# Kernel tuning notes

Measured on AMD Instinct MI355X. Metric: run time of the kernel, lower is better.

## Reference

```python
import jax, jax.numpy as jnp
import numpy as np

B, N = 2, 200
IMG = 2048
NC = 4                    # node concepts ('Is*')
NODE_CH = NC * 256        # 1024
EC = 3                    # edge concepts minus 'HigherPri'
AC = 4                    # actions
BBOX_MAX = 1024.0
E = N * (N - 1)

# static fully-connected directed edge list (src=i, dst=j, i!=j), row-major order
_ii, _jj = np.meshgrid(np.arange(N), np.arange(N), indexing='ij')
_m = _ii != _jj
SRC = jnp.asarray(_ii[_m])
DST = jnp.asarray(_jj[_m])


def _lin(k, fin, fout):
    kw, kb = jax.random.split(k)
    s = 1.0 / np.sqrt(fin)
    return (jax.random.uniform(kw, (fin, fout), jnp.float32, -s, s),
            jax.random.uniform(kb, (fout,), jnp.float32, -s, s))


def setup_inputs():
    ks = jax.random.split(jax.random.key(0), 16)
    p = {}
    p['roi_features'] = jax.random.normal(ks[0], (B, N, IMG), jnp.float32)
    p['batch_bboxes'] = jax.random.uniform(ks[1], (B, N, 4), jnp.float32) * BBOX_MAX
    p['batch_directions'] = jax.random.normal(ks[2], (B, N, 4), jnp.float32)
    p['batch_priorities'] = jax.random.normal(ks[3], (B, N), jnp.float32)
    p['w1'], p['b1'] = _lin(ks[4], IMG, 512)
    p['w2'], p['b2'] = _lin(ks[5], 512, 256)
    p['w3'], p['b3'] = _lin(ks[6], 256, NODE_CH)
    p['wi'], p['bi'] = _lin(ks[7], NODE_CH, NC)
    p['we1'], p['be1'] = _lin(ks[8], 16, 256)
    p['we2'], p['be2'] = _lin(ks[9], 256, 64)
    p['we3'], p['be3'] = _lin(ks[10], 64, EC)
    p['wp1'], p['bp1'] = _lin(ks[11], EC + 1, 128)
    p['wp2'], p['bp2'] = _lin(ks[12], 128, NODE_CH * AC)
    p['root_w'], _ = _lin(ks[13], NODE_CH, AC)
    _, p['root_b'] = _lin(ks[14], NODE_CH, AC)
    return p


def reference(roi_features, batch_bboxes, batch_directions, batch_priorities,
              w1, b1, w2, b2, w3, b3, wi, bi,
              we1, be1, we2, be2, we3, be3,
              wp1, bp1, wp2, bp2, root_w, root_b):
    # node concept embedding MLP: [B,N,IMG] -> [B,N,NODE_CH]
    h = jax.nn.relu(roi_features @ w1 + b1)
    h = jax.nn.relu(h @ w2 + b2)
    node_concepts = h @ w3 + b3
    node_concepts_explicit = jax.nn.sigmoid(node_concepts @ wi + bi)

    # pairwise attributes for all directed edges (same ordering as torch masks)
    node_attr = jnp.concatenate([batch_bboxes / BBOX_MAX, batch_directions], -1)  # [B,N,8]
    pair = jnp.concatenate([node_attr[:, SRC], node_attr[:, DST]], -1)            # [B,E,16]
    eh = jax.nn.relu(pair @ we1 + be1)
    eh = jax.nn.relu(eh @ we2 + be2)
    edge_attributes = jax.nn.sigmoid(eh @ we3 + be3)                              # [B,E,EC]
    higher_pri = (batch_priorities[:, SRC] > batch_priorities[:, DST]).astype(jnp.float32)
    edge_attributes = jnp.concatenate([edge_attributes, higher_pri[..., None]], -1)  # [B,E,EC+1]

    # NNConv on graph 0: per-edge weight matrix, gather-matmul-scatter
    x = node_concepts[0]                 # [N, NODE_CH]
    e = edge_attributes[0]               # [E, EC+1]
    w = jax.nn.relu(e @ wp1 + bp1) @ wp2 + bp2
    w = w.reshape(E, NODE_CH, AC)        # [E, NODE_CH, AC]
    msg = jnp.einsum('ei,eio->eo', x[SRC], w)          # [E, AC]
    agg = jax.ops.segment_sum(msg, DST, num_segments=N)  # [N, AC]
    next_actions = agg + x @ root_w + root_b
    return (next_actions, node_concepts_explicit[0], edge_attributes[0])
```

## Files before the change

### kernel.cpp

```cpp
#include <hip/hip_runtime.h>
#include <math.h>

#define NN 200
#define ETOT 39800

typedef float float4v __attribute__((ext_vector_type(4)));
typedef short short8 __attribute__((ext_vector_type(8)));

__device__ __forceinline__ float sigf(float x) { return 1.0f / (1.0f + expf(-x)); }

__device__ __forceinline__ unsigned short f2b(float f) {
  unsigned u = __float_as_uint(f);
  u += 0x7fffu + ((u >> 16) & 1u);
  return (unsigned short)(u >> 16);
}
__device__ __forceinline__ float b2f16(unsigned short u) {
  return __uint_as_float(((unsigned)u) << 16);
}

__global__ __launch_bounds__(256) void k_L1(
    const float* __restrict__ roi, const float* __restrict__ w1, const float* __restrict__ b1,
    const float* __restrict__ wp2, const float* __restrict__ w3,
    const float* __restrict__ wi, const float* __restrict__ rootw, const float* __restrict__ bp2,
    const float* __restrict__ b3, const float* __restrict__ w2, const float* __restrict__ we2,
    const float* __restrict__ bbox, const float* __restrict__ dir,
    const float* __restrict__ we1, const float* __restrict__ be1, const float* __restrict__ wp1,
    unsigned short* __restrict__ h1, unsigned short* __restrict__ Gm, float* __restrict__ G12f,
    float* __restrict__ Pm, float* __restrict__ Qm,
    unsigned short* __restrict__ we2T, unsigned short* __restrict__ w2T,
    float* __restrict__ wp1T, float* __restrict__ gvec, float* __restrict__ bcat) {
  __shared__ __align__(16) char sm[16640];
  const int b = blockIdx.x, tid = threadIdx.x;
  const int lane = tid & 63, wv = tid >> 6, mr = lane & 15, quad = lane >> 4;

  if (b < 416) {
    const int m0 = (b % 13) * 16, n0 = (b / 13) * 16;
    const int arow = min(m0 + mr, 199);
    const float* Ap = roi + (size_t)arow * 2048 + wv * 512 + quad * 8;
    const float* Bp0 = w1 + n0 + mr;
    float4v acc = {0.f, 0.f, 0.f, 0.f};
    for (int ks = 0; ks < 16; ++ks) {
      float4v a0 = *(const float4v*)(Ap + ks * 32);
      float4v a1 = *(const float4v*)(Ap + ks * 32 + 4);
      short8 af, bf;
      af[0]=f2b(a0[0]); af[1]=f2b(a0[1]); af[2]=f2b(a0[2]); af[3]=f2b(a0[3]);
      af[4]=f2b(a1[0]); af[5]=f2b(a1[1]); af[6]=f2b(a1[2]); af[7]=f2b(a1[3]);
      const float* Bp = Bp0 + (size_t)(wv * 512 + ks * 32 + quad * 8) * 512;
#pragma unroll
      for (int t8 = 0; t8 < 8; ++t8) bf[t8] = f2b(Bp[(size_t)t8 * 512]);
      acc = __builtin_amdgcn_mfma_f32_16x16x32_bf16(af, bf, acc, 0, 0, 0);
    }
    float (*red)[16][17] = (float (*)[16][17])sm;
#pragma unroll
    for (int r = 0; r < 4; ++r) red[wv][quad * 4 + r][mr] = acc[r];
    __syncthreads();
    const int row = tid >> 4, col = tid & 15;
    float v = red[0][row][col] + red[1][row][col] + red[2][row][col] + red[3][row][col] + b1[n0 + col];
    h1[(size_t)(m0 + row) * 512 + n0 + col] = f2b(fmaxf(v, 0.f));
  } else if (b < 928) {
    const int t = b - 416;
    const int j0 = (t % 32) * 16, c0 = (t / 32) * 16;
    const int j = j0 + mr;
    const float* Aw = wp2 + (size_t)(j >> 2) * 4096 + (j & 3);
    const float* Bp0 = w3 + (size_t)(c0 + mr) * 1024;
    float4v acc = {0.f, 0.f, 0.f, 0.f};
    for (int ks = 0; ks < 8; ++ks) {
      const int i0 = wv * 256 + ks * 32 + quad * 8;
      short8 af, bf;
#pragma unroll
      for (int t8 = 0; t8 < 8; ++t8) af[t8] = f2b(Aw[4 * (i0 + t8)]);
      float4v b0 = *(const float4v*)(Bp0 + i0);
      float4v b1v = *(const float4v*)(Bp0 + i0 + 4);
      bf[0]=f2b(b0[0]); bf[1]=f2b(b0[1]); bf[2]=f2b(b0[2]); bf[3]=f2b(b0[3]);
      bf[4]=f2b(b1v[0]); bf[5]=f2b(b1v[1]); bf[6]=f2b(b1v[2]); bf[7]=f2b(b1v[3]);
      acc = __builtin_amdgcn_mfma_f32_16x16x32_bf16(af, bf, acc, 0, 0, 0);
    }
    float (*red)[16][17] = (float (*)[16][17])sm;
#pragma unroll
    for (int r = 0; r < 4; ++r) red[wv][quad * 4 + r][mr] = acc[r];
    __syncthreads();
    const int row = tid >> 4, col = tid & 15;
    float v = red[0][row][col] + red[1][row][col] + red[2][row][col] + red[3][row][col];
    Gm[(size_t)(j0 + row) * 256 + c0 + col] = f2b(v);
  } else if (b < 1184) {
    const int c = b - 928;
    float s[12] = {};
#pragma unroll
    for (int ii = 0; ii < 4; ++ii) {
      int i = tid + ii * 256;
      float xv = w3[(size_t)c * 1024 + i];
      float4v wi4 = ((const float4v*)wi)[i];
      float4v rw4 = ((const float4v*)rootw)[i];
      float4v bp4 = ((const float4v*)bp2)[i];
#pragma unroll
      for (int q = 0; q < 4; ++q) {
        s[q] += xv * wi4[q]; s[4 + q] += xv * rw4[q]; s[8 + q] += xv * bp4[q];
      }
    }
    float (*part)[12] = (float (*)[12])sm;
#pragma unroll
    for (int r = 0; r < 12; ++r) {
      float v = s[r];
#pragma unroll
      for (int off = 32; off > 0; off >>= 1) v += __shfl_down(v, off, 64);
      if (lane == 0) part[wv][r] = v;
    }
    __syncthreads();
    if (tid < 12) G12f[c * 12 + tid] = part[0][tid] + part[1][tid] + part[2][tid] + part[3][tid];
  } else if (b < 1384) {
    const int n = b - 1184, c = tid;
    float a[8];
#pragma unroll
    for (int r = 0; r < 4; ++r) a[r] = bbox[n * 4 + r] * (1.0f / 1024.0f);
#pragma unroll
    for (int r = 0; r < 4; ++r) a[4 + r] = dir[n * 4 + r];
    float p = be1[c], q = 0.0f;
#pragma unroll
    for (int r = 0; r < 8; ++r) {
      p += a[r] * we1[r * 256 + c];
      q += a[r] * we1[(8 + r) * 256 + c];
    }
    Pm[n * 256 + c] = p;
    Qm[n * 256 + c] = q;
  } else if (b < 1400) {
    const int f = (b - 1384) * 256 + tid;
    const int c = f >> 6, k0 = (f & 63) * 4;
#pragma unroll
    for (int q = 0; q < 4; ++q)
      we2T[c * 256 + k0 + q] = f2b(we2[(k0 + q) * 64 + c]);
  } else if (b < 1432) {
    float (*lds)[65] = (float (*)[65])sm;
    const int t = b - 1400;
    const int kt = t % 8, nt = t / 8;
#pragma unroll 4
    for (int i = 0; i < 16; ++i) {
      int idx = tid + i * 256;
      int r = idx >> 6, c = idx & 63;
      lds[r][c] = w2[(size_t)(kt * 64 + r) * 256 + nt * 64 + c];
    }
    __syncthreads();
#pragma unroll 4
    for (int i = 0; i < 16; ++i) {
      int idx = tid + i * 256;
      int r = idx >> 6, c = idx & 63;
      w2T[(size_t)(nt * 64 + r) * 512 + kt * 64 + c] = f2b(lds[c][r]);
    }
  } else if (b < 1440) {
    const int j = (b - 1432) * 64 + (tid >> 2), p = tid & 3;
    const float* src = wp2 + (size_t)(j >> 2) * 4096 + (j & 3);
    float v = 0.f;
    for (int t = 0; t < 256; ++t) {
      int i = p + 4 * t;
      v += b3[i] * src[4 * i];
    }
    v += __shfl_down(v, 2, 4);
    v += __shfl_down(v, 1, 4);
    if (p == 0) gvec[j] = v;
  } else if (b == 1440) {
    if (tid < 128) {
      float4v v = {wp1[tid], wp1[128 + tid], wp1[256 + tid], wp1[384 + tid]};
      ((float4v*)wp1T)[tid] = v;
    }
  } else {
    float s[12] = {};
#pragma unroll
    for (int ii = 0; ii < 4; ++ii) {
      int i = tid + ii * 256;
      float xv = b3[i];
      float4v wi4 = ((const float4v*)wi)[i];
      float4v rw4 = ((const float4v*)rootw)[i];
      float4v bp4 = ((const float4v*)bp2)[i];
#pragma unroll
      for (int q = 0; q < 4; ++q) {
        s[q] += xv * wi4[q]; s[4 + q] += xv * rw4[q]; s[8 + q] += xv * bp4[q];
      }
    }
    float (*part)[12] = (float (*)[12])sm;
#pragma unroll
    for (int r = 0; r < 12; ++r) {
      float v = s[r];
#pragma unroll
      for (int off = 32; off > 0; off >>= 1) v += __shfl_down(v, off, 64);
      if (lane == 0) part[wv][r] = v;
    }
    __syncthreads();
    if (tid < 12) bcat[tid] = part[0][tid] + part[1][tid] + part[2][tid] + part[3][tid];
  }
}

__global__ __launch_bounds__(256) void k_L2(const unsigned short* __restrict__ h1,
                                            const unsigned short* __restrict__ w2T,
                                            const float* __restrict__ b2,
                                            unsigned short* __restrict__ h2) {
  __shared__ float red[4][16][17];
  const int tid = threadIdx.x, lane = tid & 63, wv = tid >> 6;
  const int m0 = (blockIdx.x % 13) * 16, n0 = (blockIdx.x / 13) * 16;
  const int mr = lane & 15, quad = lane >> 4;
  const unsigned short* Ap = h1 + (size_t)(m0 + mr) * 512 + wv * 128 + quad * 8;
  const unsigned short* Bp = w2T + (size_t)(n0 + mr) * 512 + wv * 128 + quad * 8;
  float4v acc = {0.f, 0.f, 0.f, 0.f};
#pragma unroll
  for (int s = 0; s < 4; ++s) {
    short8 af = *(const short8*)(Ap + s * 32);
    short8 bf = *(const short8*)(Bp + s * 32);
    acc = __builtin_amdgcn_mfma_f32_16x16x32_bf16(af, bf, acc, 0, 0, 0);
  }
#pragma unroll
  for (int r = 0; r < 4; ++r) red[wv][quad * 4 + r][mr] = acc[r];
  __syncthreads();
  const int row = tid >> 4, col = tid & 15;
  float v = red[0][row][col] + red[1][row][col] + red[2][row][col] + red[3][row][col] + b2[n0 + col];
  h2[(size_t)(m0 + row) * 256 + n0 + col] = f2b(fmaxf(v, 0.f));
}

__global__ __launch_bounds__(256) void k_L3(const unsigned short* __restrict__ h2,
                                            const unsigned short* __restrict__ Gm,
                                            const float* __restrict__ gvec,
                                            const float* __restrict__ G12f, const float* __restrict__ bcat,
                                            const float* __restrict__ bi, const float* __restrict__ rootb,
                                            float* __restrict__ Tm, float* __restrict__ out1,
                                            float* __restrict__ Um, float* __restrict__ out0) {
  __shared__ __align__(16) char sm[4352];
  const int b = blockIdx.x, tid = threadIdx.x;
  const int lane = tid & 63, wv = tid >> 6, mr = lane & 15, quad = lane >> 4;
  if (b < 416) {
    float (*red)[16][17] = (float (*)[16][17])sm;
    const int m0 = (b % 13) * 16, n0 = (b / 13) * 16;
    const unsigned short* Ap = h2 + (size_t)(m0 + mr) * 256 + wv * 64 + quad * 8;
    const unsigned short* Bp = Gm + (size_t)(n0 + mr) * 256 + wv * 64 + quad * 8;
    float4v acc = {0.f, 0.f, 0.f, 0.f};
#pragma unroll
    for (int s = 0; s < 2; ++s) {
      short8 af = *(const short8*)(Ap + s * 32);
      short8 bf = *(const short8*)(Bp + s * 32);
      acc = __builtin_amdgcn_mfma_f32_16x16x32_bf16(af, bf, acc, 0, 0, 0);
    }
#pragma unroll
    for (int r = 0; r < 4; ++r) red[wv][quad * 4 + r][mr] = acc[r];
    __syncthreads();
    const int row = tid >> 4, col = tid & 15;
    float v = red[0][row][col] + red[1][row][col] + red[2][row][col] + red[3][row][col] + gvec[n0 + col];
    Tm[(size_t)(m0 + row) * 512 + n0 + col] = v;
  } else {
    const int n = b - 416;
    const float xv = b2f16(h2[(size_t)n * 256 + tid]);
    const float4v* g4 = (const float4v*)(G12f + tid * 12);
    float s[12];
    float4v v0 = g4[0], v1 = g4[1], v2 = g4[2];
    s[0]=xv*v0[0]; s[1]=xv*v0[1]; s[2]=xv*v0[2]; s[3]=xv*v0[3];
    s[4]=xv*v1[0]; s[5]=xv*v1[1]; s[6]=xv*v1[2]; s[7]=xv*v1[3];
    s[8]=xv*v2[0]; s[9]=xv*v2[1]; s[10]=xv*v2[2]; s[11]=xv*v2[3];
    float (*part)[12] = (float (*)[12])sm;
#pragma unroll
    for (int r = 0; r < 12; ++r) {
      float v = s[r];
#pragma unroll
      for (int off = 32; off > 0; off >>= 1) v += __shfl_down(v, off, 64);
      if (lane == 0) part[wv][r] = v;
    }
    __syncthreads();
    if (tid < 12) {
      float v = part[0][tid] + part[1][tid] + part[2][tid] + part[3][tid] + bcat[tid];
      int kind = tid >> 2, c = tid & 3;
      if (kind == 0) out1[n * 4 + c] = sigf(v + bi[c]);
      else if (kind == 1) out0[n * 4 + c] = v + rootb[c];
      else Um[n * 4 + c] = v;
    }
  }
}

__global__ __launch_bounds__(256) void k_edge(
    const float* __restrict__ P, const float* __restrict__ Q,
    const unsigned short* __restrict__ we2T,
    const float* __restrict__ be2, const float* __restrict__ we3, const float* __restrict__ be3,
    const float* __restrict__ wp1T, const float* __restrict__ bp1,
    const float* __restrict__ pri,
    const float* __restrict__ T, const float* __restrict__ U,
    float* __restrict__ out0, float* __restrict__ out_ea) {
  __shared__ int src_s[64], dst_s[64];
  __shared__ float ea_s[64][4];
  __shared__ float4v wp1s[128];
  __shared__ float bp1s[128];
  __shared__ float4v Ts[2][128];
  __shared__ float Us[2][4];

  const int tid = threadIdx.x;
  const int e0 = blockIdx.x * 64;
  const int s_lo = e0 / 199;

  if (tid < 64) {
    int e = e0 + tid;
    int i = -1, j = 0;
    if (e < ETOT) {
      i = e / 199;
      int jj = e - i * 199;
      j = jj + (jj >= i ? 1 : 0);
    }
    src_s[tid] = i;
    dst_s[tid] = j;
  }
  if (tid < 128) {
    wp1s[tid] = ((const float4v*)wp1T)[tid];
    bp1s[tid] = bp1[tid];
  }
  {
    int row = tid >> 7, c = tid & 127;
    Ts[row][c] = ((const float4v*)T)[(s_lo + row) * 128 + c];
  }
  if (tid < 8) {
    int s = min(s_lo + (tid >> 2), 199);
    Us[tid >> 2][tid & 3] = U[s * 4 + (tid & 3)];
  }
  __syncthreads();

  const int lane = tid & 63;
  const int wv = tid >> 6;
  const int m = lane & 15;
  const int quad = lane >> 4;
  const int eloc = wv * 16 + m;
  const int si = src_s[eloc];
  const int dj = dst_s[eloc];

  float4v acc[4];
#pragma unroll
  for (int ct = 0; ct < 4; ++ct) { acc[ct][0] = 0.f; acc[ct][1] = 0.f; acc[ct][2] = 0.f; acc[ct][3] = 0.f; }

  const short8* W8 = (const short8*)we2T;

  for (int ks = 0; ks < 8; ++ks) {
    union { short8 s; unsigned u[4]; } af;
    af.s = (short8)0;
    if (si >= 0) {
      const float4v* p4 = (const float4v*)(P + si * 256 + ks * 32 + quad * 8);
      const float4v* q4 = (const float4v*)(Q + dj * 256 + ks * 32 + quad * 8);
      float4v v0 = p4[0] + q4[0];
      float4v v1 = p4[1] + q4[1];
      af.u[0] = (unsigned)f2b(fmaxf(v0[0], 0.f)) | ((unsigned)f2b(fmaxf(v0[1], 0.f)) << 16);
      af.u[1] = (unsigned)f2b(fmaxf(v0[2], 0.f)) | ((unsigned)f2b(fmaxf(v0[3], 0.f)) << 16);
      af.u[2] = (unsigned)f2b(fmaxf(v1[0], 0.f)) | ((unsigned)f2b(fmaxf(v1[1], 0.f)) << 16);
      af.u[3] = (unsigned)f2b(fmaxf(v1[2], 0.f)) | ((unsigned)f2b(fmaxf(v1[3], 0.f)) << 16);
    }
#pragma unroll
    for (int ct = 0; ct < 4; ++ct) {
      short8 bf = W8[(ct * 16 + m) * 32 + ks * 4 + quad];
      acc[ct] = __builtin_amdgcn_mfma_f32_16x16x32_bf16(af.s, bf, acc[ct], 0, 0, 0);
    }
  }

  float ev[4][3];
#pragma unroll
  for (int r = 0; r < 4; ++r) { ev[r][0] = 0.f; ev[r][1] = 0.f; ev[r][2] = 0.f; }
#pragma unroll
  for (int ct = 0; ct < 4; ++ct) {
    const int col = ct * 16 + m;
    const float b2v = be2[col];
    const float w0 = we3[col * 3 + 0], w1v = we3[col * 3 + 1], w2v = we3[col * 3 + 2];
#pragma unroll
    for (int r = 0; r < 4; ++r) {
      float e2 = fmaxf(acc[ct][r] + b2v, 0.f);
      ev[r][0] += e2 * w0;
      ev[r][1] += e2 * w1v;
      ev[r][2] += e2 * w2v;
    }
  }
#pragma unroll
  for (int r = 0; r < 4; ++r)
#pragma unroll
    for (int p = 0; p < 3; ++p) {
      float v = ev[r][p];
      v += __shfl_xor(v, 1, 64);
      v += __shfl_xor(v, 2, 64);
      v += __shfl_xor(v, 4, 64);
      v += __shfl_xor(v, 8, 64);
      ev[r][p] = v;
    }
  if (m == 0) {
#pragma unroll
    for (int r = 0; r < 4; ++r) {
      int el = wv * 16 + quad * 4 + r;
      int ss = src_s[el], dd = dst_s[el];
      if (ss >= 0) {
        float4v o;
        o[0] = sigf(ev[r][0] + be3[0]);
        o[1] = sigf(ev[r][1] + be3[1]);
        o[2] = sigf(ev[r][2] + be3[2]);
        o[3] = (pri[ss] > pri[dd]) ? 1.0f : 0.0f;
        *(float4v*)&ea_s[el][0] = o;
        *(float4v*)(out_ea + (size_t)(e0 + el) * 4) = o;
      }
    }
  }
  __syncthreads();

  const int ee = tid >> 2, pp = tid & 3;
  const int s2 = src_s[ee], d2 = dst_s[ee];
  float4v pm = {0.f, 0.f, 0.f, 0.f};
  if (s2 >= 0) {
    const int srow = s2 - s_lo;
    const float c0 = ea_s[ee][0], c1 = ea_s[ee][1], c2 = ea_s[ee][2], c3 = ea_s[ee][3];
#pragma unroll 8
    for (int tt = pp; tt < 128; tt += 4) {
      float4v w4 = wp1s[tt];
      float hv = bp1s[tt] + c0 * w4[0] + c1 * w4[1] + c2 * w4[2] + c3 * w4[3];
      hv = fmaxf(hv, 0.f);
      pm += hv * Ts[srow][tt];
    }
  }
#pragma unroll
  for (int o = 0; o < 4; ++o) {
    float v = pm[o];
    v += __shfl_xor(v, 1, 64);
    v += __shfl_xor(v, 2, 64);
    pm[o] = v;
  }
  if (s2 >= 0) atomicAdd(&out0[d2 * 4 + pp], Us[s2 - s_lo][pp] + pm[pp]);
}

extern "C" void kernel_launch(void* const* d_in, const int* in_sizes, int n_in,
                              void* d_out, int out_size, void* d_ws, size_t ws_size,
                              hipStream_t stream) {
  (void)in_sizes; (void)n_in; (void)out_size; (void)ws_size;
  const float* roi   = (const float*)d_in[0];
  const float* bbox  = (const float*)d_in[1];
  const float* dir   = (const float*)d_in[2];
  const float* pri   = (const float*)d_in[3];
  const float* w1    = (const float*)d_in[4];
  const float* b1    = (const float*)d_in[5];
  const float* w2    = (const float*)d_in[6];
  const float* b2    = (const float*)d_in[7];
  const float* w3    = (const float*)d_in[8];
  const float* b3    = (const float*)d_in[9];
  const float* wi    = (const float*)d_in[10];
  const float* bi    = (const float*)d_in[11];
  const float* we1   = (const float*)d_in[12];
  const float* be1   = (const float*)d_in[13];
  const float* we2   = (const float*)d_in[14];
  const float* be2   = (const float*)d_in[15];
  const float* we3   = (const float*)d_in[16];
  const float* be3   = (const float*)d_in[17];
  const float* wp1   = (const float*)d_in[18];
  const float* bp1   = (const float*)d_in[19];
  const float* wp2   = (const float*)d_in[20];
  const float* bp2   = (const float*)d_in[21];
  const float* rootw = (const float*)d_in[22];
  const float* rootb = (const float*)d_in[23];

  float* out0 = (float*)d_out;
  float* out1 = out0 + 800;
  float* out2 = out0 + 1600;

  unsigned short* us = (unsigned short*)d_ws;
  unsigned short* h1   = us;
  unsigned short* h2   = us + 106496;
  unsigned short* Gm   = us + 159744;
  unsigned short* we2T = us + 290816;
  unsigned short* w2T  = us + 307200;
  float* fb   = (float*)(us + 438272);
  float* Tm   = fb;
  float* Pm   = fb + 106496;
  float* Qm   = fb + 157696;
  float* Um   = fb + 208896;
  float* wp1T = fb + 209696;
  float* G12f = fb + 210208;
  float* gvec = fb + 213280;
  float* bcat = fb + 213792;

  k_L1<<<1442, 256, 0, stream>>>(roi, w1, b1, wp2, w3, wi, rootw, bp2, b3, w2, we2,
                                 bbox, dir, we1, be1, wp1,
                                 h1, Gm, G12f, Pm, Qm, we2T, w2T, wp1T, gvec, bcat);

  k_L2<<<208, 256, 0, stream>>>(h1, w2T, b2, h2);

  k_L3<<<616, 256, 0, stream>>>(h2, Gm, gvec, G12f, bcat, bi, rootb, Tm, out1, Um, out0);

  k_edge<<<622, 256, 0, stream>>>(Pm, Qm, we2T, be2, we3, be3, wp1T, bp1, pri, Tm, Um, out0, out2);
}
```

Measured before the change: 171.7 us.

## Pre-transpose w1 and wp2 to bf16 in a prep kernel before MFMA GEMMs

Adds a preparation kernel that transposes w1 and wp2 into contiguous bf16 layouts (w1T, WrT) alongside the existing small weight transforms. The GEMM blocks that previously did strided scalar fp32 loads with per-element bf16 conversion now do 16-byte vector loads from the transposed buffers. This removes uncoalesced strided global reads in the L1 and Gm GEMMs. In exchange it adds a kernel launch plus a write and re-read of roughly 3 MB of transposed weights every call.

```diff
diff --git a/kernel.cpp b/kernel.cpp
--- a/kernel.cpp
+++ b/kernel.cpp
@@ -18,72 +18,50 @@
   return __uint_as_float(((unsigned)u) << 16);
 }
 
-__global__ __launch_bounds__(256) void k_L1(
-    const float* __restrict__ roi, const float* __restrict__ w1, const float* __restrict__ b1,
-    const float* __restrict__ wp2, const float* __restrict__ w3,
-    const float* __restrict__ wi, const float* __restrict__ rootw, const float* __restrict__ bp2,
-    const float* __restrict__ b3, const float* __restrict__ w2, const float* __restrict__ we2,
+__global__ __launch_bounds__(256) void k_prep(
+    const float* __restrict__ w1, const float* __restrict__ w2, const float* __restrict__ wp2,
+    const float* __restrict__ w3, const float* __restrict__ wi, const float* __restrict__ rootw,
+    const float* __restrict__ bp2, const float* __restrict__ b3, const float* __restrict__ we2,
     const float* __restrict__ bbox, const float* __restrict__ dir,
     const float* __restrict__ we1, const float* __restrict__ be1, const float* __restrict__ wp1,
-    unsigned short* __restrict__ h1, unsigned short* __restrict__ Gm, float* __restrict__ G12f,
-    float* __restrict__ Pm, float* __restrict__ Qm,
-    unsigned short* __restrict__ we2T, unsigned short* __restrict__ w2T,
-    float* __restrict__ wp1T, float* __restrict__ gvec, float* __restrict__ bcat) {
+    unsigned short* __restrict__ w1T, unsigned short* __restrict__ w2T,
+    unsigned short* __restrict__ WrT, unsigned short* __restrict__ we2T,
+    float* __restrict__ G12f, float* __restrict__ Pm, float* __restrict__ Qm,
+    float* __restrict__ gvec, float* __restrict__ wp1T, float* __restrict__ bcat) {
   __shared__ __align__(16) char sm[16640];
   const int b = blockIdx.x, tid = threadIdx.x;
-  const int lane = tid & 63, wv = tid >> 6, mr = lane & 15, quad = lane >> 4;
-
-  if (b < 416) {
-    const int m0 = (b % 13) * 16, n0 = (b / 13) * 16;
-    const int arow = min(m0 + mr, 199);
-    const float* Ap = roi + (size_t)arow * 2048 + wv * 512 + quad * 8;
-    const float* Bp0 = w1 + n0 + mr;
-    float4v acc = {0.f, 0.f, 0.f, 0.f};
-    for (int ks = 0; ks < 16; ++ks) {
-      float4v a0 = *(const float4v*)(Ap + ks * 32);
-      float4v a1 = *(const float4v*)(Ap + ks * 32 + 4);
-      short8 af, bf;
-      af[0]=f2b(a0[0]); af[1]=f2b(a0[1]); af[2]=f2b(a0[2]); af[3]=f2b(a0[3]);
-      af[4]=f2b(a1[0]); af[5]=f2b(a1[1]); af[6]=f2b(a1[2]); af[7]=f2b(a1[3]);
-      const float* Bp = Bp0 + (size_t)(wv * 512 + ks * 32 + quad * 8) * 512;
-#pragma unroll
-      for (int t8 = 0; t8 < 8; ++t8) bf[t8] = f2b(Bp[(size_t)t8 * 512]);
-      acc = __builtin_amdgcn_mfma_f32_16x16x32_bf16(af, bf, acc, 0, 0, 0);
-    }
-    float (*red)[16][17] = (float (*)[16][17])sm;
-#pragma unroll
-    for (int r = 0; r < 4; ++r) red[wv][quad * 4 + r][mr] = acc[r];
-    __syncthreads();
-    const int row = tid >> 4, col = tid & 15;
-    float v = red[0][row][col] + red[1][row][col] + red[2][row][col] + red[3][row][col] + b1[n0 + col];
-    h1[(size_t)(m0 + row) * 512 + n0 + col] = f2b(fmaxf(v, 0.f));
-  } else if (b < 928) {
-    const int t = b - 416;
-    const int j0 = (t % 32) * 16, c0 = (t / 32) * 16;
-    const int j = j0 + mr;
-    const float* Aw = wp2 + (size_t)(j >> 2) * 4096 + (j & 3);
-    const float* Bp0 = w3 + (size_t)(c0 + mr) * 1024;
-    float4v acc = {0.f, 0.f, 0.f, 0.f};
-    for (int ks = 0; ks < 8; ++ks) {
-      const int i0 = wv * 256 + ks * 32 + quad * 8;
-      short8 af, bf;
-#pragma unroll
-      for (int t8 = 0; t8 < 8; ++t8) af[t8] = f2b(Aw[4 * (i0 + t8)]);
-      float4v b0 = *(const float4v*)(Bp0 + i0);
-      float4v b1v = *(const float4v*)(Bp0 + i0 + 4);
-      bf[0]=f2b(b0[0]); bf[1]=f2b(b0[1]); bf[2]=f2b(b0[2]); bf[3]=f2b(b0[3]);
-      bf[4]=f2b(b1v[0]); bf[5]=f2b(b1v[1]); bf[6]=f2b(b1v[2]); bf[7]=f2b(b1v[3]);
-      acc = __builtin_amdgcn_mfma_f32_16x16x32_bf16(af, bf, acc, 0, 0, 0);
-    }
-    float (*red)[16][17] = (float (*)[16][17])sm;
-#pragma unroll
-    for (int r = 0; r < 4; ++r) red[wv][quad * 4 + r][mr] = acc[r];
-    __syncthreads();
-    const int row = tid >> 4, col = tid & 15;
-    float v = red[0][row][col] + red[1][row][col] + red[2][row][col] + red[3][row][col];
-    Gm[(size_t)(j0 + row) * 256 + c0 + col] = f2b(v);
-  } else if (b < 1184) {
-    const int c = b - 928;
+  const int lane = tid & 63, wv = tid >> 6;
+
+  if (b < 288) {
+    float (*lds)[65] = (float (*)[65])sm;
+    const float* Wf;
+    unsigned short* Wt;
+    int K, N, t;
+    if (b < 256) { Wf = w1; Wt = w1T; K = 2048; N = 512; t = b; }
+    else { Wf = w2; Wt = w2T; K = 512; N = 256; t = b - 256; }
+    const int K64 = K >> 6;
+    const int kt = t % K64, nt = t / K64;
+#pragma unroll 4
+    for (int i = 0; i < 16; ++i) {
+      int idx = tid + i * 256;
+      int r = idx >> 6, c = idx & 63;
+      lds[r][c] = Wf[(size_t)(kt * 64 + r) * N + nt * 64 + c];
+    }
+    __syncthreads();
+#pragma unroll 4
+    for (int i = 0; i < 16; ++i) {
+      int idx = tid + i * 256;
+      int r = idx >> 6, c = idx & 63;
+      Wt[(size_t)(nt * 64 + r) * K + kt * 64 + c] = f2b(lds[c][r]);
+    }
+  } else if (b < 416) {
+    int k = b - 288;
+    int o = tid >> 6, l = tid & 63;
+    const float* src = wp2 + (size_t)k * 4096;
+    unsigned short* dst = WrT + (size_t)(k * 4 + o) * 1024;
+    for (int i = l; i < 1024; i += 64) dst[i] = f2b(src[i * 4 + o]);
+  } else if (b < 672) {
+    const int c = b - 416;
     float s[12] = {};
 #pragma unroll
     for (int ii = 0; ii < 4; ++ii) {
@@ -107,8 +85,8 @@
     }
     __syncthreads();
     if (tid < 12) G12f[c * 12 + tid] = part[0][tid] + part[1][tid] + part[2][tid] + part[3][tid];
-  } else if (b < 1384) {
-    const int n = b - 1184, c = tid;
+  } else if (b < 872) {
+    const int n = b - 672, c = tid;
     float a[8];
 #pragma unroll
     for (int r = 0; r < 4; ++r) a[r] = bbox[n * 4 + r] * (1.0f / 1024.0f);
@@ -122,31 +100,14 @@
     }
     Pm[n * 256 + c] = p;
     Qm[n * 256 + c] = q;
-  } else if (b < 1400) {
-    const int f = (b - 1384) * 256 + tid;
+  } else if (b < 888) {
+    const int f = (b - 872) * 256 + tid;
     const int c = f >> 6, k0 = (f & 63) * 4;
 #pragma unroll
     for (int q = 0; q < 4; ++q)
       we2T[c * 256 + k0 + q] = f2b(we2[(k0 + q) * 64 + c]);
-  } else if (b < 1432) {
-    float (*lds)[65] = (float (*)[65])sm;
-    const int t = b - 1400;
-    const int kt = t % 8, nt = t / 8;
-#pragma unroll 4
-    for (int i = 0; i < 16; ++i) {
-      int idx = tid + i * 256;
-      int r = idx >> 6, c = idx & 63;
-      lds[r][c] = w2[(size_t)(kt * 64 + r) * 256 + nt * 64 + c];
-    }
-    __syncthreads();
-#pragma unroll 4
-    for (int i = 0; i < 16; ++i) {
-      int idx = tid + i * 256;
-      int r = idx >> 6, c = idx & 63;
-      w2T[(size_t)(nt * 64 + r) * 512 + kt * 64 + c] = f2b(lds[c][r]);
-    }
-  } else if (b < 1440) {
-    const int j = (b - 1432) * 64 + (tid >> 2), p = tid & 3;
+  } else if (b < 896) {
+    const int j = (b - 888) * 64 + (tid >> 2), p = tid & 3;
     const float* src = wp2 + (size_t)(j >> 2) * 4096 + (j & 3);
     float v = 0.f;
     for (int t = 0; t < 256; ++t) {
@@ -156,7 +117,7 @@
     v += __shfl_down(v, 2, 4);
     v += __shfl_down(v, 1, 4);
     if (p == 0) gvec[j] = v;
-  } else if (b == 1440) {
+  } else if (b == 896) {
     if (tid < 128) {
       float4v v = {wp1[tid], wp1[128 + tid], wp1[256 + tid], wp1[384 + tid]};
       ((float4v*)wp1T)[tid] = v;
@@ -188,7 +149,60 @@
   }
 }
 
-__global__ __launch_bounds__(256) void k_L2(const unsigned short* __restrict__ h1,
+__global__ __launch_bounds__(256) void k_mid(
+    const float* __restrict__ roi, const unsigned short* __restrict__ w1T, const float* __restrict__ b1,
+    const unsigned short* __restrict__ WrT, const float* __restrict__ w3,
+    unsigned short* __restrict__ h1, unsigned short* __restrict__ Gm) {
+  __shared__ float red[4][16][17];
+  const int b = blockIdx.x, tid = threadIdx.x;
+  const int lane = tid & 63, wv = tid >> 6, mr = lane & 15, quad = lane >> 4;
+
+  if (b < 416) {
+    const int m0 = (b % 13) * 16, n0 = (b / 13) * 16;
+    const int arow = min(m0 + mr, 199);
+    const float* Ap = roi + (size_t)arow * 2048 + wv * 512 + quad * 8;
+    const unsigned short* Bp = w1T + (size_t)(n0 + mr) * 2048 + wv * 512 + quad * 8;
+    float4v acc = {0.f, 0.f, 0.f, 0.f};
+    for (int ks = 0; ks < 16; ++ks) {
+      float4v a0 = *(const float4v*)(Ap + ks * 32);
+      float4v a1 = *(const float4v*)(Ap + ks * 32 + 4);
+      short8 af;
+      af[0]=f2b(a0[0]); af[1]=f2b(a0[1]); af[2]=f2b(a0[2]); af[3]=f2b(a0[3]);
+      af[4]=f2b(a1[0]); af[5]=f2b(a1[1]); af[6]=f2b(a1[2]); af[7]=f2b(a1[3]);
+      short8 bf = *(const short8*)(Bp + ks * 32);
+      acc = __builtin_amdgcn_mfma_f32_16x16x32_bf16(af, bf, acc, 0, 0, 0);
+    }
+#pragma unroll
+    for (int r = 0; r < 4; ++r) red[wv][quad * 4 + r][mr] = acc[r];
+    __syncthreads();
+    const int row = tid >> 4, col = tid & 15;
+    float v = red[0][row][col] + red[1][row][col] + red[2][row][col] + red[3][row][col] + b1[n0 + col];
+    h1[(size_t)(m0 + row) * 512 + n0 + col] = f2b(fmaxf(v, 0.f));
+  } else {
+    const int t = b - 416;
+    const int j0 = (t % 32) * 16, c0 = (t / 32) * 16;
+    const unsigned short* Ap = WrT + (size_t)(j0 + mr) * 1024 + wv * 256 + quad * 8;
+    const float* Bp = w3 + (size_t)(c0 + mr) * 1024 + wv * 256 + quad * 8;
+    float4v acc = {0.f, 0.f, 0.f, 0.f};
+    for (int ks = 0; ks < 8; ++ks) {
+      short8 af = *(const short8*)(Ap + ks * 32);
+      float4v b0 = *(const float4v*)(Bp + ks * 32);
+      float4v b1v = *(const float4v*)(Bp + ks * 32 + 4);
+      short8 bf;
+      bf[0]=f2b(b0[0]); bf[1]=f2b(b0[1]); bf[2]=f2b(b0[2]); bf[3]=f2b(b0[3]);
+      bf[4]=f2b(b1v[0]); bf[5]=f2b(b1v[1]); bf[6]=f2b(b1v[2]); bf[7]=f2b(b1v[3]);
+      acc = __builtin_amdgcn_mfma_f32_16x16x32_bf16(af, bf, acc, 0, 0, 0);
+    }
+#pragma unroll
+    for (int r = 0; r < 4; ++r) red[wv][quad * 4 + r][mr] = acc[r];
+    __syncthreads();
+    const int row = tid >> 4, col = tid & 15;
+    float v = red[0][row][col] + red[1][row][col] + red[2][row][col] + red[3][row][col];
+    Gm[(size_t)(j0 + row) * 256 + c0 + col] = f2b(v);
+  }
+}
+
+__global__ __launch_bounds__(256) void k_h2(const unsigned short* __restrict__ h1,
                                             const unsigned short* __restrict__ w2T,
                                             const float* __restrict__ b2,
                                             unsigned short* __restrict__ h2) {
@@ -213,7 +227,7 @@
   h2[(size_t)(m0 + row) * 256 + n0 + col] = f2b(fmaxf(v, 0.f));
 }
 
-__global__ __launch_bounds__(256) void k_L3(const unsigned short* __restrict__ h2,
+__global__ __launch_bounds__(256) void k_TN(const unsigned short* __restrict__ h2,
                                             const unsigned short* __restrict__ Gm,
                                             const float* __restrict__ gvec,
                                             const float* __restrict__ G12f, const float* __restrict__ bcat,
@@ -450,12 +464,14 @@
   float* out2 = out0 + 1600;
 
   unsigned short* us = (unsigned short*)d_ws;
-  unsigned short* h1   = us;
-  unsigned short* h2   = us + 106496;
-  unsigned short* Gm   = us + 159744;
-  unsigned short* we2T = us + 290816;
-  unsigned short* w2T  = us + 307200;
-  float* fb   = (float*)(us + 438272);
+  unsigned short* w1T  = us;
+  unsigned short* w2T  = us + 1048576;
+  unsigned short* WrT  = us + 1179648;
+  unsigned short* we2T = us + 1703936;
+  unsigned short* h1   = us + 1720320;
+  unsigned short* h2   = us + 1826816;
+  unsigned short* Gm   = us + 1880064;
+  float* fb   = (float*)(us + 2011136);
   float* Tm   = fb;
   float* Pm   = fb + 106496;
   float* Qm   = fb + 157696;
@@ -465,13 +481,15 @@
   float* gvec = fb + 213280;
   float* bcat = fb + 213792;
 
-  k_L1<<<1442, 256, 0, stream>>>(roi, w1, b1, wp2, w3, wi, rootw, bp2, b3, w2, we2,
-                                 bbox, dir, we1, be1, wp1,
-                                 h1, Gm, G12f, Pm, Qm, we2T, w2T, wp1T, gvec, bcat);
-
-  k_L2<<<208, 256, 0, stream>>>(h1, w2T, b2, h2);
-
-  k_L3<<<616, 256, 0, stream>>>(h2, Gm, gvec, G12f, bcat, bi, rootb, Tm, out1, Um, out0);
+  k_prep<<<898, 256, 0, stream>>>(w1, w2, wp2, w3, wi, rootw, bp2, b3, we2,
+                                  bbox, dir, we1, be1, wp1,
+                                  w1T, w2T, WrT, we2T, G12f, Pm, Qm, gvec, wp1T, bcat);
+
+  k_mid<<<928, 256, 0, stream>>>(roi, w1T, b1, WrT, w3, h1, Gm);
+
+  k_h2<<<208, 256, 0, stream>>>(h1, w2T, b2, h2);
+
+  k_TN<<<616, 256, 0, stream>>>(h2, Gm, gvec, G12f, bcat, bi, rootb, Tm, out1, Um, out0);
 
   k_edge<<<622, 256, 0, stream>>>(Pm, Qm, we2T, be2, we3, be3, wp1T, bp1, pri, Tm, Um, out0, out2);
 }
```

New measurement: 175.5 us. +2.2%, slower.
